# Kernel optimization log

Measured on AMD Instinct MI355X. Metric: run time of the kernel, lower is better.

The kernel has to match this reference:

```python
import jax, jax.numpy as jnp
import numpy as np

THRESH = 0.5      # jaccard_thresh
NEGPOS = 3        # neg:pos ratio for hard negative mining
VAR0, VAR1 = 0.1, 0.2  # SSD encoding variances


def point_form(boxes):
    # center-size [P,4] -> (xmin,ymin,xmax,ymax)
    return jnp.concatenate([boxes[:, :2] - boxes[:, 2:] / 2,
                            boxes[:, :2] + boxes[:, 2:] / 2], axis=1)


def jaccard(box_a, box_b):
    # box_a [O,4], box_b [P,4] point-form -> IoU [O,P]
    lt = jnp.maximum(box_a[:, None, :2], box_b[None, :, :2])
    rb = jnp.minimum(box_a[:, None, 2:], box_b[None, :, 2:])
    wh = jnp.clip(rb - lt, 0.0)
    inter = wh[..., 0] * wh[..., 1]
    area_a = ((box_a[:, 2] - box_a[:, 0]) * (box_a[:, 3] - box_a[:, 1]))[:, None]
    area_b = ((box_b[:, 2] - box_b[:, 0]) * (box_b[:, 3] - box_b[:, 1]))[None, :]
    return inter / (area_a + area_b - inter)


def encode(matched, priors):
    # matched point-form [P,4], priors center-size [P,4]
    g_cxcy = ((matched[:, :2] + matched[:, 2:]) / 2 - priors[:, :2]) / (VAR0 * priors[:, 2:])
    g_wh = jnp.log((matched[:, 2:] - matched[:, :2]) / priors[:, 2:]) / VAR1
    return jnp.concatenate([g_cxcy, g_wh], axis=1)


def match_one(truths, labels, priors):
    # truths [O,4] point-form, labels [O] int, priors [P,4] center-size
    O = truths.shape[0]
    ov = jaccard(truths, point_form(priors))          # [O,P]
    best_prior_idx = jnp.argmax(ov, axis=1)           # [O]
    best_truth_ov = jnp.max(ov, axis=0)               # [P]
    best_truth_idx = jnp.argmax(ov, axis=0)           # [P]
    # ensure each gt matches its best prior
    best_truth_ov = best_truth_ov.at[best_prior_idx].set(2.0)
    best_truth_idx = best_truth_idx.at[best_prior_idx].set(jnp.arange(O))
    matches = truths[best_truth_idx]                  # [P,4]
    conf = jnp.where(best_truth_ov < THRESH, 0, labels[best_truth_idx] + 1)
    return encode(matches, priors), conf


def setup_inputs() -> dict:
    key = jax.random.key(0)
    ks = jax.random.split(key, 6)
    B, P, C, O = 32, 24656, 81, 16
    predictions = jax.random.normal(ks[0], (B, P, 4 + C), dtype=jnp.float32)
    # priors: center-size, valid w/h
    pc = jax.random.uniform(ks[1], (P, 2), minval=0.05, maxval=0.95)
    pwh = jax.random.uniform(ks[2], (P, 2), minval=0.02, maxval=0.3)
    priors = jnp.concatenate([pc, pwh], axis=1).astype(jnp.float32)
    # ground-truth boxes in point form, guaranteed positive extent
    tc = jax.random.uniform(ks[3], (B, O, 2), minval=0.2, maxval=0.8)
    twh = jax.random.uniform(ks[4], (B, O, 2), minval=0.05, maxval=0.3)
    targets_boxes = jnp.concatenate([tc - twh / 2, tc + twh / 2], axis=-1).astype(jnp.float32)
    targets_labels = jax.random.randint(ks[5], (B, O), 0, C - 1, dtype=jnp.int32)
    return {"predictions": predictions, "targets_boxes": targets_boxes,
            "targets_labels": targets_labels, "priors": priors}


def reference(predictions, targets_boxes, targets_labels, priors):
    loc_data = predictions[..., :4]        # [B,P,4]
    conf_data = predictions[..., 4:]       # [B,P,C]
    B, P = loc_data.shape[:2]
    C = conf_data.shape[2]

    loc_t, conf_t = jax.vmap(match_one, in_axes=(0, 0, None))(
        targets_boxes, targets_labels, priors)   # [B,P,4], [B,P]

    pos = conf_t > 0                                   # [B,P]
    # smooth L1 on positives, sum reduction
    d = loc_data - loc_t
    ad = jnp.abs(d)
    sl1 = jnp.where(ad < 1.0, 0.5 * d * d, ad - 0.5)
    loss_l = jnp.sum(sl1 * pos[..., None].astype(sl1.dtype))

    # per-anchor cross entropy
    logp = jax.nn.log_softmax(conf_data, axis=-1)
    lbl = jnp.clip(conf_t, 0, C - 1)
    ce = -jnp.take_along_axis(logp, lbl[..., None], axis=-1)[..., 0]  # [B,P]

    # hard negative mining: rank negatives by loss (positives zeroed)
    loss_rank = jnp.where(pos, 0.0, ce)
    loss_idx = jnp.argsort(-loss_rank, axis=1)
    idx_rank = jnp.argsort(loss_idx, axis=1)
    num_pos = jnp.sum(pos, axis=1, keepdims=True)          # [B,1]
    num_neg = jnp.minimum(num_pos * NEGPOS, P)
    neg = idx_rank < num_neg

    sel = (pos | neg).astype(ce.dtype)
    loss_c = jnp.sum(ce * sel)

    N = jnp.sum(num_pos).astype(loss_l.dtype)
    return loss_l / N, loss_c / N
```

## Files before the change

kernel.cpp:

```cpp
#include <hip/hip_runtime.h>
#include <math.h>

#define NB 32
#define NP 24656
#define NO 16
#define NC 81
#define ND 85
#define THRESH_F 0.5f
#define NEGPOS_I 3
#define VAR0_F 0.1f
#define VAR1_F 0.2f
#define NEG_HUGE -1e30f

#define BPCNT (NB * NP)
#define MBLK2 25
#define CHB 386
#define SPB 24
#define CBYTES 22528

typedef unsigned long long u64;

__global__ __launch_bounds__(256) void k_match(
    const float* __restrict__ tboxes, const float* __restrict__ priors,
    float2* __restrict__ bt2, u64* __restrict__ mcand,
    int* __restrict__ npos, float* __restrict__ accB, int* __restrict__ done) {
    const int b = blockIdx.y, bx = blockIdx.x, tid = threadIdx.x;
    const int lane = tid & 63, wv = tid >> 6;
    __shared__ float tb[NO * 4];
    __shared__ u64 wkey[4][NO];
    if (bx == 0 && b == 0) {
        if (tid < NB) npos[tid] = 0;
        if (tid < 2 * NB) accB[tid] = 0.f;
        if (tid == 0) *done = 0;
    }
    if (tid < NO * 4) tb[tid] = tboxes[b * NO * 4 + tid];
    __syncthreads();

    const int p0 = bx * 1024 + tid * 4;
    float pl[4], pt[4], prr[4], pbm[4], pa[4];
    bool pv[4];
#pragma unroll
    for (int j = 0; j < 4; ++j) {
        const int p = p0 + j;
        pv[j] = (p < NP);
        const float4 q = pv[j] ? ((const float4*)priors)[p]
                               : make_float4(0.f, 0.f, 1.f, 1.f);
        pl[j] = q.x - q.z * 0.5f; pt[j] = q.y - q.w * 0.5f;
        prr[j] = q.x + q.z * 0.5f; pbm[j] = q.y + q.w * 0.5f;
        pa[j] = (prr[j] - pl[j]) * (pbm[j] - pt[j]);
    }
    float bestv[4] = {-1.f, -1.f, -1.f, -1.f};
    int besti[4] = {0, 0, 0, 0};
    for (int o = 0; o < NO; ++o) {
        const float al = tb[o * 4], at = tb[o * 4 + 1];
        const float ar = tb[o * 4 + 2], ab = tb[o * 4 + 3];
        const float aarea = (ar - al) * (ab - at);
        u64 kmax = 0ull;
#pragma unroll
        for (int j = 0; j < 4; ++j) {
            float iw = fminf(ar, prr[j]) - fmaxf(al, pl[j]); iw = fmaxf(iw, 0.f);
            float ih = fminf(ab, pbm[j]) - fmaxf(at, pt[j]); ih = fmaxf(ih, 0.f);
            const float inter = iw * ih;
            const float iou = inter / (aarea + pa[j] - inter);
            if (pv[j]) {
                if (iou > bestv[j]) { bestv[j] = iou; besti[j] = o; }
                const u64 key = ((u64)__float_as_uint(iou) << 32) |
                                (u64)(0xFFFFFFFFu - (unsigned)(p0 + j));
                kmax = (key > kmax) ? key : kmax;
            }
        }
        for (int d = 1; d < 64; d <<= 1) {
            const u64 other = __shfl_xor(kmax, d, 64);
            kmax = (other > kmax) ? other : kmax;
        }
        if (lane == 0) wkey[wv][o] = kmax;
    }
#pragma unroll
    for (int j = 0; j < 4; ++j)
        if (pv[j])
            bt2[(size_t)b * NP + p0 + j] =
                make_float2(bestv[j], __int_as_float(besti[j]));
    __syncthreads();
    if (tid < NO) {
        u64 k0 = wkey[0][tid];
        k0 = (wkey[1][tid] > k0) ? wkey[1][tid] : k0;
        k0 = (wkey[2][tid] > k0) ? wkey[2][tid] : k0;
        k0 = (wkey[3][tid] > k0) ? wkey[3][tid] : k0;
        mcand[((size_t)(b * NO + tid)) * MBLK2 + bx] = k0;
    }
}

__device__ __forceinline__ void stage_chunk(const char* __restrict__ gpred,
                                            int b, int r0, char* ldsbuf,
                                            int lane) {
    const size_t off = ((size_t)b * NP + r0) * (size_t)(ND * 4);
    const char* g = gpred + off;
    const bool unsafe = (b == NB - 1) && (r0 + 64 > NP);
    if (!unsafe) {
#pragma unroll
        for (int k = 0; k < 22; ++k)
            __builtin_amdgcn_global_load_lds(
                (const __attribute__((address_space(1))) void*)(g + k * 1024 +
                                                               lane * 16),
                (__attribute__((address_space(3))) void*)(ldsbuf + k * 1024),
                16, 0, 0);
    } else {
        const int nf4 = (NP - r0) * ND / 4;
        const float4* gs = (const float4*)g;
        float4* ld = (float4*)ldsbuf;
        for (int i = lane; i < nf4; i += 64) ld[i] = gs[i];
    }
}

__global__ __launch_bounds__(64) void k_main(
    const float* __restrict__ pred, const float* __restrict__ tboxes,
    const int* __restrict__ tlabels, const float* __restrict__ priors,
    const float2* __restrict__ bt2, const u64* __restrict__ mcand,
    float* __restrict__ lr, int* __restrict__ npos, float* __restrict__ accB) {
    __shared__ float4 smem[2][CBYTES / 16];

    const int b = blockIdx.y;
    const int span = blockIdx.x;
    const int lane = threadIdx.x;
    const size_t bbase = (size_t)b * NP;
    const char* gpred = (const char*)pred;

    char* cur = (char*)smem[0];
    char* nxt = (char*)smem[1];

    const int Ab = 16 * (21 * lane + (lane >> 2));
    const int c0 = lane & 3;

    u64 pbk = 0ull;
    if (lane < NO) {
        const u64* c = mcand + (size_t)(b * NO + lane) * MBLK2;
        for (int i = 0; i < MBLK2; ++i) {
            const u64 v = c[i];
            pbk = (v > pbk) ? v : pbk;
        }
    }
    int p16[NO];
#pragma unroll
    for (int j = 0; j < NO; ++j) {
        const u64 kj = __shfl(pbk, j, 64);
        p16[j] = (int)(0xFFFFFFFFu - (unsigned)(kj & 0xFFFFFFFFull));
    }

    float my_ll = 0.f, my_ce = 0.f;
    int my_np = 0;

    int chunk = span;
    if (chunk < CHB) stage_chunk(gpred, b, chunk * 64, cur, lane);
    int next_chunk = chunk + SPB;

    while (chunk < CHB) {
        if (next_chunk < CHB) {
            stage_chunk(gpred, b, next_chunk * 64, nxt, lane);
            asm volatile("s_waitcnt vmcnt(22)" ::: "memory");
        } else {
            asm volatile("s_waitcnt vmcnt(0)" ::: "memory");
        }

        const int r0 = chunk * 64;
        const int nrows = min(64, NP - r0);

        float4 v[22];
#pragma unroll
        for (int k = 0; k < 22; ++k)
            v[k] = *(const float4*)(cur + Ab + 16 * k);

        const float bg = (c0 == 0) ? v[1].x : (c0 == 1) ? v[1].y
                       : (c0 == 2) ? v[1].z : v[1].w;
        float4 h = v[1];
        h.x = (c0 >= 1) ? NEG_HUGE : h.x;
        h.y = (c0 >= 2) ? NEG_HUGE : h.y;
        h.z = (c0 >= 3) ? NEG_HUGE : h.z;
        float4 t4 = v[21];
        t4.y = (c0 < 1) ? NEG_HUGE : t4.y;
        t4.z = (c0 < 2) ? NEG_HUGE : t4.z;
        t4.w = (c0 < 3) ? NEG_HUGE : t4.w;

        float4 MA = h, MB = t4;
#pragma unroll
        for (int k = 2; k < 21; k += 2) {
            MA.x = fmaxf(MA.x, v[k].x); MA.y = fmaxf(MA.y, v[k].y);
            MA.z = fmaxf(MA.z, v[k].z); MA.w = fmaxf(MA.w, v[k].w);
        }
#pragma unroll
        for (int k = 3; k < 21; k += 2) {
            MB.x = fmaxf(MB.x, v[k].x); MB.y = fmaxf(MB.y, v[k].y);
            MB.z = fmaxf(MB.z, v[k].z); MB.w = fmaxf(MB.w, v[k].w);
        }
        const float m = fmaxf(fmaxf(fmaxf(MA.x, MB.x), fmaxf(MA.y, MB.y)),
                              fmaxf(fmaxf(MA.z, MB.z), fmaxf(MA.w, MB.w)));

        float sA = __expf(h.x - m) + __expf(h.y - m) +
                   __expf(h.z - m) + __expf(h.w - m);
        float sB = __expf(t4.x - m) + __expf(t4.y - m) +
                   __expf(t4.z - m) + __expf(t4.w - m);
#pragma unroll
        for (int k = 2; k < 21; k += 2)
            sA += __expf(v[k].x - m) + __expf(v[k].y - m) +
                  __expf(v[k].z - m) + __expf(v[k].w - m);
#pragma unroll
        for (int k = 3; k < 21; k += 2)
            sB += __expf(v[k].x - m) + __expf(v[k].y - m) +
                  __expf(v[k].z - m) + __expf(v[k].w - m);
        const float lse = m + __logf(sA + sB);

        if (lane < nrows) {
            const int p = r0 + lane;
            const float2 bt = bt2[bbase + p];
            int o_f = -1;
#pragma unroll
            for (int j = 0; j < NO; ++j)
                if (p == p16[j]) o_f = j;
            const bool forced = (o_f >= 0);
            const bool pos = forced || (bt.x >= THRESH_F);
            const int o = forced ? o_f : __float_as_int(bt.y);
            lr[bbase + p] = pos ? 0.f : (lse - bg);
            if (pos) {
                my_np += 1;
                const int lbl = tlabels[b * NO + o] + 1;
                const float val = *(const float*)(cur + 340 * lane + (4 + lbl) * 4);
                my_ce += lse - val;
                const float4 pq = *((const float4*)priors + p);
                const float tx0 = tboxes[(b * NO + o) * 4 + 0];
                const float ty0 = tboxes[(b * NO + o) * 4 + 1];
                const float tx1 = tboxes[(b * NO + o) * 4 + 2];
                const float ty1 = tboxes[(b * NO + o) * 4 + 3];
                const float l0 = (c0 == 0) ? v[0].x : (c0 == 1) ? v[0].y
                               : (c0 == 2) ? v[0].z : v[0].w;
                const float l1 = (c0 == 0) ? v[0].y : (c0 == 1) ? v[0].z
                               : (c0 == 2) ? v[0].w : v[1].x;
                const float l2 = (c0 == 0) ? v[0].z : (c0 == 1) ? v[0].w
                               : (c0 == 2) ? v[1].x : v[1].y;
                const float l3 = (c0 == 0) ? v[0].w : (c0 == 1) ? v[1].x
                               : (c0 == 2) ? v[1].y : v[1].z;
                const float g0 = ((tx0 + tx1) * 0.5f - pq.x) / (VAR0_F * pq.z);
                const float g1 = ((ty0 + ty1) * 0.5f - pq.y) / (VAR0_F * pq.w);
                const float g2 = __logf((tx1 - tx0) / pq.z) / VAR1_F;
                const float g3 = __logf((ty1 - ty0) / pq.w) / VAR1_F;
                float dd, ad;
                dd = l0 - g0; ad = fabsf(dd); my_ll += (ad < 1.f) ? 0.5f * dd * dd : (ad - 0.5f);
                dd = l1 - g1; ad = fabsf(dd); my_ll += (ad < 1.f) ? 0.5f * dd * dd : (ad - 0.5f);
                dd = l2 - g2; ad = fabsf(dd); my_ll += (ad < 1.f) ? 0.5f * dd * dd : (ad - 0.5f);
                dd = l3 - g3; ad = fabsf(dd); my_ll += (ad < 1.f) ? 0.5f * dd * dd : (ad - 0.5f);
            }
        }
        chunk = next_chunk;
        next_chunk += SPB;
        char* tmp = cur; cur = nxt; nxt = tmp;
    }

    for (int d2 = 1; d2 < 64; d2 <<= 1) {
        my_ll += __shfl_xor(my_ll, d2, 64);
        my_ce += __shfl_xor(my_ce, d2, 64);
        my_np += __shfl_xor(my_np, d2, 64);
    }
    if (lane == 0) {
        if (my_ll != 0.f) atomicAdd(&accB[b * 2 + 0], my_ll);
        if (my_ce != 0.f) atomicAdd(&accB[b * 2 + 1], my_ce);
        if (my_np) atomicAdd(&npos[b], my_np);
    }
}

__global__ __launch_bounds__(1024) void k_select(
    const float* __restrict__ lrk, const int* __restrict__ npos,
    float* __restrict__ accB, int* __restrict__ done, float* __restrict__ out) {
    const int b = blockIdx.x;
    const float* row = lrk + (size_t)b * NP;
    const int tid = threadIdx.x;
    const int lane = tid & 63;
    const int wid = tid >> 6;

    __shared__ unsigned hist[2048];
    __shared__ int sh_bucket, sh_knew;
    __shared__ float wsum[16];
    __shared__ int wcnt[16];

    const int K0 = min(npos[b] * NEGPOS_I, NP);
    int k = K0;
    unsigned prefix = 0;

    const int shifts[3] = {21, 10, 0};
    const unsigned masks[3] = {0u, 0xFFE00000u, 0xFFFFFC00u};

    for (int pass = 0; pass < 3; ++pass) {
        const int shift = shifts[pass];
        const unsigned mask_hi = masks[pass];
        hist[tid] = 0;
        hist[tid + 1024] = 0;
        __syncthreads();
        for (int i = tid; i < NP; i += 1024) {
            const unsigned v = __float_as_uint(row[i]);
            if ((v & mask_hi) == (prefix & mask_hi))
                atomicAdd(&hist[(v >> shift) & 2047u], 1u);
        }
        __syncthreads();
        if (tid < 64) {
            unsigned g = 0;
            for (int j = 0; j < 32; ++j) g += hist[lane * 32 + j];
            unsigned T = g;
            for (int d = 1; d < 64; d <<= 1) {
                const unsigned t = __shfl_down(T, d, 64);
                if (lane + d < 64) T += t;
            }
            const unsigned E = T - g;
            const bool hit = (E < (unsigned)k) && ((unsigned)k <= T);
            const unsigned long long msk = __ballot(hit);
            const int wl = __ffsll(msk) - 1;
            if (lane == wl) {
                unsigned cum = E;
                int bsel = lane * 32, kn = k;
                for (int j = 31; j >= 0; --j) {
                    const unsigned c = hist[lane * 32 + j];
                    if (cum + c >= (unsigned)k) {
                        bsel = lane * 32 + j;
                        kn = k - (int)cum;
                        break;
                    }
                    cum += c;
                }
                sh_bucket = bsel;
                sh_knew = kn;
            }
        }
        __syncthreads();
        prefix |= ((unsigned)sh_bucket) << shift;
        k = sh_knew;
        __syncthreads();
    }
    const float T = __uint_as_float(prefix);

    float msum = 0.f;
    int mcnt = 0;
    for (int i = tid; i < NP; i += 1024) {
        const float v = row[i];
        if (__float_as_uint(v) > prefix) { msum += v; mcnt++; }
    }
    for (int s = 32; s > 0; s >>= 1) {
        msum += __shfl_down(msum, s, 64);
        mcnt += __shfl_down(mcnt, s, 64);
    }
    if (lane == 0) { wsum[wid] = msum; wcnt[wid] = mcnt; }
    __syncthreads();
    if (tid == 0) {
        float tot = 0.f;
        int cnt = 0;
        for (int w = 0; w < 16; ++w) { tot += wsum[w]; cnt += wcnt[w]; }
        atomicAdd(&accB[b * 2 + 1], tot + (float)(K0 - cnt) * T);
        __threadfence();
        if (atomicAdd(done, 1) == NB - 1) {
            volatile const float* va = accB;
            volatile const int* vn = npos;
            int n = 0;
            float a0 = 0.f, a1 = 0.f;
            for (int bb = 0; bb < NB; ++bb) {
                n += vn[bb];
                a0 += va[bb * 2 + 0];
                a1 += va[bb * 2 + 1];
            }
            const float N = (float)n;
            out[0] = a0 / N;
            out[1] = a1 / N;
        }
    }
}

extern "C" void kernel_launch(void* const* d_in, const int* in_sizes, int n_in,
                              void* d_out, int out_size, void* d_ws, size_t ws_size,
                              hipStream_t stream) {
    const float* pred   = (const float*)d_in[0];
    const float* tboxes = (const float*)d_in[1];
    const int*   tlabels = (const int*)d_in[2];
    const float* priors = (const float*)d_in[3];
    float* out = (float*)d_out;

    char* w = (char*)d_ws;
    float2* bt2 = (float2*)w;
    float*  lrk = (float*)(w + 8ull * BPCNT);
    u64*    mcand = (u64*)(w + 12ull * BPCNT);
    char*   w2 = w + 12ull * BPCNT + 8ull * NB * NO * MBLK2;
    int*    npos = (int*)w2;
    float*  accB = (float*)(w2 + 4ull * NB);
    int*    done = (int*)(w2 + 4ull * NB + 8ull * NB);

    k_match<<<dim3(MBLK2, NB), dim3(256), 0, stream>>>(
        tboxes, priors, bt2, mcand, npos, accB, done);
    k_main<<<dim3(SPB, NB), dim3(64), 0, stream>>>(
        pred, tboxes, tlabels, priors, bt2, mcand, lrk, npos, accB);
    k_select<<<dim3(NB), dim3(1024), 0, stream>>>(lrk, npos, accB, done, out);
}
```

Measured before the change: 124.0 us.

## Split each row across two lanes with 32-row chunks and more blocks

The main loss kernel now processes 32-row chunks, with each anchor row handled by a lane pair. Each lane reduces half of the 81 logits, and the max and sum are combined with a shuffle. The grid grows from 24 to 56 blocks per batch and the LDS double buffer halves, which raises occupancy and per-row parallelism for the log-sum-exp. Loc values and the label logit are now read straight from LDS instead of being selected from registers. In exchange, half of each lane pair idles in the positive-anchor branch, and there are twice as many chunk iterations with extra shuffles.

```diff
diff --git a/kernel.cpp b/kernel.cpp
--- a/kernel.cpp
+++ b/kernel.cpp
@@ -14,9 +14,9 @@
 
 #define BPCNT (NB * NP)
 #define MBLK2 25
-#define CHB 386
-#define SPB 24
-#define CBYTES 22528
+#define CHB32 771
+#define SPB2 56
+#define CB32 11264
 
 typedef unsigned long long u64;
 
@@ -90,15 +90,15 @@
     }
 }
 
-__device__ __forceinline__ void stage_chunk(const char* __restrict__ gpred,
-                                            int b, int r0, char* ldsbuf,
-                                            int lane) {
-    const size_t off = ((size_t)b * NP + r0) * (size_t)(ND * 4);
+__device__ __forceinline__ void stage32(const char* __restrict__ gpred,
+                                        int b, int r0, char* ldsbuf,
+                                        int lane) {
+    const size_t off = ((size_t)b * NP + r0) * 340ull;
     const char* g = gpred + off;
-    const bool unsafe = (b == NB - 1) && (r0 + 64 > NP);
+    const bool unsafe = (b == NB - 1) && (r0 + 34 > NP);
     if (!unsafe) {
 #pragma unroll
-        for (int k = 0; k < 22; ++k)
+        for (int k = 0; k < 11; ++k)
             __builtin_amdgcn_global_load_lds(
                 (const __attribute__((address_space(1))) void*)(g + k * 1024 +
                                                                lane * 16),
@@ -117,7 +117,7 @@
     const int* __restrict__ tlabels, const float* __restrict__ priors,
     const float2* __restrict__ bt2, const u64* __restrict__ mcand,
     float* __restrict__ lr, int* __restrict__ npos, float* __restrict__ accB) {
-    __shared__ float4 smem[2][CBYTES / 16];
+    __shared__ char smem[2][CB32];
 
     const int b = blockIdx.y;
     const int span = blockIdx.x;
@@ -125,11 +125,14 @@
     const size_t bbase = (size_t)b * NP;
     const char* gpred = (const char*)pred;
 
-    char* cur = (char*)smem[0];
-    char* nxt = (char*)smem[1];
-
-    const int Ab = 16 * (21 * lane + (lane >> 2));
-    const int c0 = lane & 3;
+    char* cur = smem[0];
+    char* nxt = smem[1];
+
+    const int rho = lane >> 1;
+    const int h = lane & 1;
+    const int c0 = rho & 3;
+    const int Ab = 16 * (21 * rho + (rho >> 2));
+    const int sbase = h ? 11 : 1;
 
     u64 pbk = 0ull;
     if (lane < NO) {
@@ -150,66 +153,64 @@
     int my_np = 0;
 
     int chunk = span;
-    if (chunk < CHB) stage_chunk(gpred, b, chunk * 64, cur, lane);
-    int next_chunk = chunk + SPB;
-
-    while (chunk < CHB) {
-        if (next_chunk < CHB) {
-            stage_chunk(gpred, b, next_chunk * 64, nxt, lane);
-            asm volatile("s_waitcnt vmcnt(22)" ::: "memory");
+    stage32(gpred, b, chunk * 32, cur, lane);
+    int next_chunk = chunk + SPB2;
+
+    while (chunk < CHB32) {
+        if (next_chunk < CHB32) {
+            stage32(gpred, b, next_chunk * 32, nxt, lane);
+            asm volatile("s_waitcnt vmcnt(11)" ::: "memory");
         } else {
             asm volatile("s_waitcnt vmcnt(0)" ::: "memory");
         }
 
-        const int r0 = chunk * 64;
-        const int nrows = min(64, NP - r0);
-
-        float4 v[22];
-#pragma unroll
-        for (int k = 0; k < 22; ++k)
-            v[k] = *(const float4*)(cur + Ab + 16 * k);
-
-        const float bg = (c0 == 0) ? v[1].x : (c0 == 1) ? v[1].y
-                       : (c0 == 2) ? v[1].z : v[1].w;
-        float4 h = v[1];
-        h.x = (c0 >= 1) ? NEG_HUGE : h.x;
-        h.y = (c0 >= 2) ? NEG_HUGE : h.y;
-        h.z = (c0 >= 3) ? NEG_HUGE : h.z;
-        float4 t4 = v[21];
-        t4.y = (c0 < 1) ? NEG_HUGE : t4.y;
-        t4.z = (c0 < 2) ? NEG_HUGE : t4.z;
-        t4.w = (c0 < 3) ? NEG_HUGE : t4.w;
-
-        float4 MA = h, MB = t4;
-#pragma unroll
-        for (int k = 2; k < 21; k += 2) {
-            MA.x = fmaxf(MA.x, v[k].x); MA.y = fmaxf(MA.y, v[k].y);
-            MA.z = fmaxf(MA.z, v[k].z); MA.w = fmaxf(MA.w, v[k].w);
-        }
-#pragma unroll
-        for (int k = 3; k < 21; k += 2) {
-            MB.x = fmaxf(MB.x, v[k].x); MB.y = fmaxf(MB.y, v[k].y);
-            MB.z = fmaxf(MB.z, v[k].z); MB.w = fmaxf(MB.w, v[k].w);
-        }
-        const float m = fmaxf(fmaxf(fmaxf(MA.x, MB.x), fmaxf(MA.y, MB.y)),
-                              fmaxf(fmaxf(MA.z, MB.z), fmaxf(MA.w, MB.w)));
-
-        float sA = __expf(h.x - m) + __expf(h.y - m) +
-                   __expf(h.z - m) + __expf(h.w - m);
-        float sB = __expf(t4.x - m) + __expf(t4.y - m) +
-                   __expf(t4.z - m) + __expf(t4.w - m);
-#pragma unroll
-        for (int k = 2; k < 21; k += 2)
-            sA += __expf(v[k].x - m) + __expf(v[k].y - m) +
-                  __expf(v[k].z - m) + __expf(v[k].w - m);
-#pragma unroll
-        for (int k = 3; k < 21; k += 2)
-            sB += __expf(v[k].x - m) + __expf(v[k].y - m) +
-                  __expf(v[k].z - m) + __expf(v[k].w - m);
-        const float lse = m + __logf(sA + sB);
-
-        if (lane < nrows) {
-            const int p = r0 + lane;
+        const int r0 = chunk * 32;
+        const int nrows = min(32, NP - r0);
+
+        float4 v[11];
+#pragma unroll
+        for (int k = 0; k < 11; ++k)
+            v[k] = *(const float4*)(cur + Ab + 16 * (sbase + k));
+
+        float vals[44];
+#pragma unroll
+        for (int k = 0; k < 11; ++k) {
+            const float xs[4] = {v[k].x, v[k].y, v[k].z, v[k].w};
+#pragma unroll
+            for (int t = 0; t < 4; ++t) {
+                bool ok;
+                if (k == 0)
+                    ok = h ? false : (t >= c0);
+                else if (k == 10)
+                    ok = h ? (t <= c0) : true;
+                else
+                    ok = true;
+                vals[4 * k + t] = ok ? xs[t] : NEG_HUGE;
+            }
+        }
+        float mA = vals[0], mB = vals[1];
+#pragma unroll
+        for (int j = 2; j < 44; j += 2) {
+            mA = fmaxf(mA, vals[j]);
+            mB = fmaxf(mB, vals[j + 1]);
+        }
+        float m = fmaxf(mA, mB);
+        m = fmaxf(m, __shfl_xor(m, 1, 64));
+
+        float sA = 0.f, sB = 0.f;
+#pragma unroll
+        for (int j = 0; j < 44; j += 2) {
+            sA += __expf(vals[j] - m);
+            sB += __expf(vals[j + 1] - m);
+        }
+        float ssum = sA + sB;
+        ssum += __shfl_xor(ssum, 1, 64);
+        const float lse = m + __logf(ssum);
+
+        if (h == 0 && rho < nrows) {
+            const float bg = (c0 == 0) ? v[0].x : (c0 == 1) ? v[0].y
+                           : (c0 == 2) ? v[0].z : v[0].w;
+            const int p = r0 + rho;
             const float2 bt = bt2[bbase + p];
             int o_f = -1;
 #pragma unroll
@@ -221,35 +222,27 @@
             lr[bbase + p] = pos ? 0.f : (lse - bg);
             if (pos) {
                 my_np += 1;
+                const float* rowp = (const float*)(cur + 340 * rho);
                 const int lbl = tlabels[b * NO + o] + 1;
-                const float val = *(const float*)(cur + 340 * lane + (4 + lbl) * 4);
-                my_ce += lse - val;
+                my_ce += lse - rowp[4 + lbl];
                 const float4 pq = *((const float4*)priors + p);
                 const float tx0 = tboxes[(b * NO + o) * 4 + 0];
                 const float ty0 = tboxes[(b * NO + o) * 4 + 1];
                 const float tx1 = tboxes[(b * NO + o) * 4 + 2];
                 const float ty1 = tboxes[(b * NO + o) * 4 + 3];
-                const float l0 = (c0 == 0) ? v[0].x : (c0 == 1) ? v[0].y
-                               : (c0 == 2) ? v[0].z : v[0].w;
-                const float l1 = (c0 == 0) ? v[0].y : (c0 == 1) ? v[0].z
-                               : (c0 == 2) ? v[0].w : v[1].x;
-                const float l2 = (c0 == 0) ? v[0].z : (c0 == 1) ? v[0].w
-                               : (c0 == 2) ? v[1].x : v[1].y;
-                const float l3 = (c0 == 0) ? v[0].w : (c0 == 1) ? v[1].x
-                               : (c0 == 2) ? v[1].y : v[1].z;
                 const float g0 = ((tx0 + tx1) * 0.5f - pq.x) / (VAR0_F * pq.z);
                 const float g1 = ((ty0 + ty1) * 0.5f - pq.y) / (VAR0_F * pq.w);
                 const float g2 = __logf((tx1 - tx0) / pq.z) / VAR1_F;
                 const float g3 = __logf((ty1 - ty0) / pq.w) / VAR1_F;
                 float dd, ad;
-                dd = l0 - g0; ad = fabsf(dd); my_ll += (ad < 1.f) ? 0.5f * dd * dd : (ad - 0.5f);
-                dd = l1 - g1; ad = fabsf(dd); my_ll += (ad < 1.f) ? 0.5f * dd * dd : (ad - 0.5f);
-                dd = l2 - g2; ad = fabsf(dd); my_ll += (ad < 1.f) ? 0.5f * dd * dd : (ad - 0.5f);
-                dd = l3 - g3; ad = fabsf(dd); my_ll += (ad < 1.f) ? 0.5f * dd * dd : (ad - 0.5f);
+                dd = rowp[0] - g0; ad = fabsf(dd); my_ll += (ad < 1.f) ? 0.5f * dd * dd : (ad - 0.5f);
+                dd = rowp[1] - g1; ad = fabsf(dd); my_ll += (ad < 1.f) ? 0.5f * dd * dd : (ad - 0.5f);
+                dd = rowp[2] - g2; ad = fabsf(dd); my_ll += (ad < 1.f) ? 0.5f * dd * dd : (ad - 0.5f);
+                dd = rowp[3] - g3; ad = fabsf(dd); my_ll += (ad < 1.f) ? 0.5f * dd * dd : (ad - 0.5f);
             }
         }
         chunk = next_chunk;
-        next_chunk += SPB;
+        next_chunk += SPB2;
         char* tmp = cur; cur = nxt; nxt = tmp;
     }
 
@@ -388,7 +381,7 @@
 
     k_match<<<dim3(MBLK2, NB), dim3(256), 0, stream>>>(
         tboxes, priors, bt2, mcand, npos, accB, done);
-    k_main<<<dim3(SPB, NB), dim3(64), 0, stream>>>(
+    k_main<<<dim3(SPB2, NB), dim3(64), 0, stream>>>(
         pred, tboxes, tlabels, priors, bt2, mcand, lrk, npos, accB);
     k_select<<<dim3(NB), dim3(1024), 0, stream>>>(lrk, npos, accB, done, out);
 }
```

Result: no change. 124.0 us (+0.0%).
